# Kernel optimization log

Hardware: AMD Instinct MI355X
Metric: run time of the kernel (lower is better)

Reference implementation:

```python
import jax, jax.numpy as jnp
import numpy as np

B, L, HID = 1, 2048, 4096
H, KV, D = 32, 2, 128
ROT = int(D * 0.5)  # partial rotary dims per head
THETA = 10000.0
SCALE = D ** -0.5


def _rope_tables(L, rot, theta):
    inv_freq = 1.0 / (theta ** (np.arange(0, rot, 2, dtype=np.float32) / rot))  # [rot/2]
    t = np.arange(L, dtype=np.float32)
    freqs = np.outer(t, inv_freq)  # [L, rot/2]
    return jnp.asarray(np.cos(freqs)), jnp.asarray(np.sin(freqs))


def setup_inputs() -> dict:
    key = jax.random.key(0)
    ks = jax.random.split(key, 8)
    s = HID ** -0.5
    x = jax.random.normal(ks[0], (B, L, HID), dtype=jnp.float32)
    Wq = jax.random.normal(ks[1], (HID, H * D), dtype=jnp.float32) * s
    Wk = jax.random.normal(ks[2], (HID, KV * D), dtype=jnp.float32) * s
    Wv = jax.random.normal(ks[3], (HID, KV * D), dtype=jnp.float32) * s
    Wo = jax.random.normal(ks[4], (H * D, HID), dtype=jnp.float32) * s
    bq = jax.random.normal(ks[5], (H * D,), dtype=jnp.float32) * 0.01
    bk = jax.random.normal(ks[6], (KV * D,), dtype=jnp.float32) * 0.01
    bv = jax.random.normal(ks[7], (KV * D,), dtype=jnp.float32) * 0.01
    cos, sin = _rope_tables(L, ROT, THETA)
    # additive causal mask
    causal = jnp.tril(jnp.ones((L, L), dtype=bool))
    attention_mask = jnp.where(causal, 0.0, -1e9)[None, None].astype(jnp.float32)
    return {"x": x, "Wq": Wq, "bq": bq, "Wk": Wk, "bk": bk, "Wv": Wv, "bv": bv,
            "Wo": Wo, "cos": cos, "sin": sin, "attention_mask": attention_mask}


def _apply_rope(t, cos, sin):
    # t: [B, h, L, D]; rotary on first ROT dims, pass-through on the rest
    t_rot, t_pass = t[..., :ROT], t[..., ROT:]
    x1, x2 = t_rot[..., : ROT // 2], t_rot[..., ROT // 2:]
    c = cos[None, None]  # [1,1,L,ROT/2]
    s = sin[None, None]
    rot = jnp.concatenate([x1 * c - x2 * s, x2 * c + x1 * s], axis=-1)
    return jnp.concatenate([rot, t_pass], axis=-1)


def reference(x, Wq, bq, Wk, bk, Wv, bv, Wo, cos, sin, attention_mask):
    Bx, Lx, _ = x.shape
    q = (x @ Wq + bq).reshape(Bx, Lx, H, D).transpose(0, 2, 1, 3)   # [B,H,L,D]
    k = (x @ Wk + bk).reshape(Bx, Lx, KV, D).transpose(0, 2, 1, 3)  # [B,KV,L,D]
    v = (x @ Wv + bv).reshape(Bx, Lx, KV, D).transpose(0, 2, 1, 3)
    q = _apply_rope(q, cos, sin)
    k = _apply_rope(k, cos, sin)
    # GQA: repeat KV heads
    rep = H // KV
    k = jnp.repeat(k, rep, axis=1)  # [B,H,L,D]
    v = jnp.repeat(v, rep, axis=1)
    w = jnp.einsum('bhqd,bhkd->bhqk', q, k) * SCALE + attention_mask
    w = jax.nn.softmax(w, axis=-1)
    o = jnp.einsum('bhqk,bhkd->bhqd', w, v)
    o = o.transpose(0, 2, 1, 3).reshape(Bx, Lx, H * D)
    return o @ Wo
```

## Files before the change

kernel.cpp:

```cpp
#include <hip/hip_runtime.h>
#include <stdint.h>

#define L_SEQ 2048
#define HID   4096
#define NH    32
#define NKV   2
#define DH    128
#define NQKV  4608
#define QSCALE 0.088388347648318447f

typedef __bf16 bf16x8 __attribute__((ext_vector_type(8)));
typedef float  f32x4  __attribute__((ext_vector_type(4)));

__device__ __forceinline__ unsigned short f2bf(float f) {
  union { float f; unsigned u; } cv; cv.f = f;
  unsigned u = cv.u;
  return (unsigned short)((u + 0x7fffu + ((u >> 16) & 1u)) >> 16);
}
__device__ __forceinline__ float bf2f(unsigned short h) {
  union { unsigned u; float f; } cv; cv.u = (unsigned)h << 16; return cv.f;
}
__device__ __forceinline__ unsigned pk2(float a, float b) {
  return (unsigned)f2bf(a) | ((unsigned)f2bf(b) << 16);
}

#define GLL16(gsrc, ldst)                                                              \
  __builtin_amdgcn_global_load_lds(                                                    \
      (const __attribute__((address_space(1))) unsigned int*)(gsrc),                   \
      (__attribute__((address_space(3))) unsigned int*)(ldst), 16, 0, 0)

__device__ __forceinline__ void transpose_tile(const float* __restrict__ in,
                                               unsigned short* __restrict__ out,
                                               int R, int C, int bx, int by,
                                               float* tile , int tid) {
  const int c0 = bx * 64, r0 = by * 64;
  #pragma unroll
  for (int it = 0; it < 4; ++it) {
    int row = it * 16 + (tid >> 4);
    float4 v = *reinterpret_cast<const float4*>(&in[(size_t)(r0 + row) * C + c0 + (tid & 15) * 4]);
    tile[row * 65 + (tid & 15) * 4 + 0] = v.x;
    tile[row * 65 + (tid & 15) * 4 + 1] = v.y;
    tile[row * 65 + (tid & 15) * 4 + 2] = v.z;
    tile[row * 65 + (tid & 15) * 4 + 3] = v.w;
  }
  __syncthreads();
  #pragma unroll
  for (int it = 0; it < 8; ++it) {
    int c  = it * 8 + (tid >> 5);
    int rp = tid & 31;
    unsigned u = (unsigned)f2bf(tile[2 * rp * 65 + c]) |
                 ((unsigned)f2bf(tile[(2 * rp + 1) * 65 + c]) << 16);
    *reinterpret_cast<unsigned*>(&out[(size_t)(c0 + c) * R + r0 + 2 * rp]) = u;
  }
}

__global__ __launch_bounds__(256) void preproc_kernel(const float* __restrict__ x,
                                                      unsigned short* __restrict__ xb,
                                                      const float* __restrict__ Wq,
                                                      const float* __restrict__ Wk,
                                                      const float* __restrict__ Wv,
                                                      unsigned short* __restrict__ Wqkvt) {
  __shared__ __attribute__((aligned(16))) float tile[64 * 65];
  const int tid = threadIdx.x;
  int bid = blockIdx.x;
  if (bid < 8192) {
    int i = bid * 256 + tid;
    float4 v = reinterpret_cast<const float4*>(x)[i];
    ushort4 o;
    o.x = f2bf(v.x); o.y = f2bf(v.y); o.z = f2bf(v.z); o.w = f2bf(v.w);
    reinterpret_cast<ushort4*>(xb)[i] = o;
    return;
  }
  bid -= 8192;
  if (bid < 4096) {
    transpose_tile(Wq, Wqkvt, HID, HID, bid & 63, bid >> 6, tile, tid);
  } else if (bid < 4352) {
    bid -= 4096;
    transpose_tile(Wk, Wqkvt + (size_t)4096 * HID, HID, 256, bid & 3, bid >> 2, tile, tid);
  } else {
    bid -= 4352;
    transpose_tile(Wv, Wqkvt + (size_t)4352 * HID, HID, 256, bid & 3, bid >> 2, tile, tid);
  }
}

__global__ __launch_bounds__(256) void vtrans_kernel(const unsigned short* __restrict__ in,
                                                     unsigned short* __restrict__ out) {
  __shared__ unsigned short tile[64][72];
  const int l0 = blockIdx.x * 64, d0 = blockIdx.y * 64, g = blockIdx.z;
  const int tid = threadIdx.x;
  #pragma unroll
  for (int it = 0; it < 2; ++it) {
    int l = it * 32 + (tid >> 3);
    *reinterpret_cast<uint4*>(&tile[l][(tid & 7) * 8]) =
        *reinterpret_cast<const uint4*>(&in[((size_t)g * L_SEQ + l0 + l) * DH + d0 + (tid & 7) * 8]);
  }
  __syncthreads();
  #pragma unroll
  for (int it = 0; it < 2; ++it) {
    int d = it * 32 + (tid >> 3);
    unsigned short tmp[8];
    #pragma unroll
    for (int e = 0; e < 8; ++e) tmp[e] = tile[(tid & 7) * 8 + e][d];
    *reinterpret_cast<uint4*>(&out[((size_t)g * DH + d0 + d) * L_SEQ + l0 + (tid & 7) * 8]) =
        *reinterpret_cast<uint4*>(tmp);
  }
}

#define TBM 128
#define TBN 128
#define TBK 32

template <int MODE>
__global__ __launch_bounds__(256, 4) void gemm128_kernel(const unsigned short* __restrict__ A,
                                                         const unsigned short* __restrict__ Bt,
                                                         float* __restrict__ C,
                                                         const float* __restrict__ bq,
                                                         const float* __restrict__ bk,
                                                         const float* __restrict__ bv,
                                                         const float* __restrict__ cosT,
                                                         const float* __restrict__ sinT,
                                                         unsigned short* __restrict__ qb,
                                                         unsigned short* __restrict__ kb,
                                                         unsigned short* __restrict__ vlin,
                                                         const float* __restrict__ Wo,
                                                         unsigned short* __restrict__ Wot,
                                                         int M, int N, int K) {
  __shared__ __attribute__((aligned(16))) unsigned short smem[2 * TBM * TBK + 2 * TBN * TBK];
  const int tid = threadIdx.x;
  const int gx = N >> 7;
  const int nwgg = (M >> 7) * gx;
  const int flat = blockIdx.x;

  if (MODE == 1 && flat >= nwgg) {
    int tb = flat - nwgg;
    transpose_tile(Wo, Wot, HID, HID, tb & 63, tb >> 6,
                   reinterpret_cast<float*>(smem), tid);
    return;
  }

  unsigned short* Asb = smem;
  unsigned short* Bsb = smem + 2 * TBM * TBK;
  const int wave = tid >> 6, lane = tid & 63;
  const int lg = lane >> 4, ll = lane & 15;
  const int wm = wave >> 1, wn = wave & 1;

  int bx = flat % gx, by = flat / gx;
  if ((nwgg & 7) == 0) {
    int t = (flat & 7) * (nwgg >> 3) + (flat >> 3);
    bx = t % gx; by = t / gx;
  }
  const int m0 = by * TBM, n0 = bx * TBN;

  f32x4 acc[4][4] = {};
  const int NT = K >> 5;

  auto stage = [&](int t, int buf) {
    const int k0 = t * TBK;
    #pragma unroll
    for (int i = 0; i < 2; ++i) {
      int ci  = (i * 4 + wave) * 64 + lane;
      int row = ci >> 2;
      int cg  = (ci & 3) ^ ((row >> 1) & 3);
      GLL16(A + (size_t)(m0 + row) * K + k0 + cg * 8, &Asb[buf * TBM * TBK + (i * 4 + wave) * 512]);
    }
    #pragma unroll
    for (int i = 0; i < 2; ++i) {
      int ci  = (i * 4 + wave) * 64 + lane;
      int row = ci >> 2;
      int cg  = (ci & 3) ^ ((row >> 1) & 3);
      GLL16(Bt + (size_t)(n0 + row) * K + k0 + cg * 8, &Bsb[buf * TBN * TBK + (i * 4 + wave) * 512]);
    }
  };

  stage(0, 0);
  stage(1, 1);

  for (int t = 0; t < NT; ++t) {
    const int cur = t & 1;
    if (t + 1 < NT) asm volatile("s_waitcnt vmcnt(4)" ::: "memory");
    else            asm volatile("s_waitcnt vmcnt(0)" ::: "memory");
    __builtin_amdgcn_s_barrier();

    const unsigned short* Ac = &Asb[cur * TBM * TBK];
    const unsigned short* Bc = &Bsb[cur * TBN * TBK];
    bf16x8 afr[4], bfr[4];
    #pragma unroll
    for (int i = 0; i < 4; ++i) {
      int ra = wm * 64 + i * 16 + ll;
      afr[i] = *reinterpret_cast<const bf16x8*>(
          &Ac[ra * 32 + ((lg ^ ((ra >> 1) & 3)) * 8)]);
      int rb = wn * 64 + i * 16 + ll;
      bfr[i] = *reinterpret_cast<const bf16x8*>(
          &Bc[rb * 32 + ((lg ^ ((rb >> 1) & 3)) * 8)]);
    }
    asm volatile("s_waitcnt lgkmcnt(0)" ::: "memory");
    __builtin_amdgcn_s_barrier();
    if (t + 2 < NT) stage(t + 2, cur);

    __builtin_amdgcn_s_setprio(1);
    #pragma unroll
    for (int i = 0; i < 4; ++i)
      #pragma unroll
      for (int j = 0; j < 4; ++j)
        acc[i][j] = __builtin_amdgcn_mfma_f32_16x16x32_bf16(afr[i], bfr[j], acc[i][j], 0, 0, 0);
    __builtin_amdgcn_s_setprio(0);
  }

  if (MODE == 0) {
    #pragma unroll
    for (int i = 0; i < 4; ++i)
      #pragma unroll
      for (int j = 0; j < 4; ++j) {
        int col  = n0 + wn * 64 + j * 16 + ll;
        int rowb = m0 + wm * 64 + i * 16 + lg * 4;
        #pragma unroll
        for (int r = 0; r < 4; ++r)
          C[(size_t)(rowb + r) * N + col] = acc[i][j][r];
      }
  } else {
    const int region = (n0 < 4096) ? 0 : ((n0 < 4352) ? 1 : 2);
    const int hh = (region == 0) ? (n0 >> 7) : ((region == 1) ? ((n0 - 4096) >> 7) : ((n0 - 4352) >> 7));
    const float* bias = (region == 0) ? bq : ((region == 1) ? bk : bv);
    #pragma unroll
    for (int j = 0; j < 4; ++j) {
      float bj = bias[hh * DH + wn * 64 + j * 16 + ll];
      #pragma unroll
      for (int i = 0; i < 4; ++i)
        #pragma unroll
        for (int r = 0; r < 4; ++r) acc[i][j][r] += bj;
    }
    if (region < 2 && wn == 0) {
      #pragma unroll
      for (int i = 0; i < 4; ++i)
        #pragma unroll
        for (int r = 0; r < 4; ++r) {
          int l = m0 + wm * 64 + i * 16 + lg * 4 + r;
          float c0 = cosT[l * 32 + ll],      s0 = sinT[l * 32 + ll];
          float c1 = cosT[l * 32 + 16 + ll], s1 = sinT[l * 32 + 16 + ll];
          float x10 = acc[i][0][r], x20 = acc[i][2][r];
          float x11 = acc[i][1][r], x21 = acc[i][3][r];
          acc[i][0][r] = x10 * c0 - x20 * s0;
          acc[i][2][r] = x20 * c0 + x10 * s0;
          acc[i][1][r] = x11 * c1 - x21 * s1;
          acc[i][3][r] = x21 * c1 + x11 * s1;
        }
    }
    const float scale = (region == 0) ? QSCALE : 1.f;
    unsigned short* dst = (region == 0) ? qb : ((region == 1) ? kb : vlin);
    #pragma unroll
    for (int i = 0; i < 4; ++i)
      #pragma unroll
      for (int j = 0; j < 4; ++j) {
        int d = wn * 64 + j * 16 + ll;
        #pragma unroll
        for (int r = 0; r < 4; ++r) {
          int l = m0 + wm * 64 + i * 16 + lg * 4 + r;
          dst[((size_t)hh * L_SEQ + l) * DH + d] = f2bf(acc[i][j][r] * scale);
        }
      }
  }
}

__global__ __launch_bounds__(256, 2) void attn_kernel(const unsigned short* __restrict__ qg,
                                                      const unsigned short* __restrict__ kb,
                                                      const unsigned short* __restrict__ vt,
                                                      unsigned short* __restrict__ ob) {
  __shared__ __attribute__((aligned(16))) unsigned short Ks[2][64 * 128];
  __shared__ __attribute__((aligned(16))) unsigned short Vs[2][128 * 64];

  const int pair = blockIdx.x, h = blockIdx.y;
  const int g = h >> 4;
  const int tid = threadIdx.x, wave = tid >> 6, lane = tid & 63;
  const int lg = lane >> 4, ll = lane & 15;

  const int krow = (lane >> 4);
  const int kcg0 = (lane & 15);
  const int vrow = (lane >> 3);
  const int vcg0 = (lane & 7);

  #pragma unroll
  for (int seg = 0; seg < 2; ++seg) {
    const int qt = seg ? (31 - pair) : pair;
    const int q0 = qt * 64 + wave * 16;

    bf16x8 qf[4];
    #pragma unroll
    for (int f = 0; f < 4; ++f)
      qf[f] = *reinterpret_cast<const bf16x8*>(
          qg + ((size_t)h * L_SEQ + q0 + ll) * DH + f * 32 + lg * 8);

    f32x4 of[8] = {};
    float m = -1e30f, lsum = 0.f;

    const int kvN = qt + 1;
    int cur = 0;

    #pragma unroll
    for (int c = 0; c < 4; ++c) {
      int issue = wave * 4 + c;
      int rk = issue * 4 + krow;
      GLL16(kb + ((size_t)g * L_SEQ + rk) * DH + (kcg0 ^ (rk & 7)) * 8, &Ks[0][issue * 512]);
      int rv = issue * 8 + vrow;
      GLL16(vt + ((size_t)g * DH + rv) * L_SEQ + (vcg0 ^ (rv & 7)) * 8, &Vs[0][issue * 512]);
    }
    __syncthreads();

    for (int t = 0; t < kvN; ++t) {
      if (t + 1 < kvN) {
        int kv1 = (t + 1) * 64;
        #pragma unroll
        for (int c = 0; c < 4; ++c) {
          int issue = wave * 4 + c;
          int rk = issue * 4 + krow;
          GLL16(kb + ((size_t)g * L_SEQ + kv1 + rk) * DH + (kcg0 ^ (rk & 7)) * 8,
                &Ks[cur ^ 1][issue * 512]);
          int rv = issue * 8 + vrow;
          GLL16(vt + ((size_t)g * DH + rv) * L_SEQ + kv1 + (vcg0 ^ (rv & 7)) * 8,
                &Vs[cur ^ 1][issue * 512]);
        }
      }

      f32x4 s[4] = {};
      const unsigned short* Kc = &Ks[cur][0];
      #pragma unroll
      for (int cf = 0; cf < 4; ++cf) {
        bf16x8 kf[4];
        #pragma unroll
        for (int f = 0; f < 4; ++f) {
          int rk = cf * 16 + ll;
          int cc = (f * 4 + lg) ^ (rk & 7);
          kf[f] = *reinterpret_cast<const bf16x8*>(&Kc[rk * 128 + cc * 8]);
        }
        __builtin_amdgcn_s_setprio(1);
        #pragma unroll
        for (int f = 0; f < 4; ++f)
          s[cf] = __builtin_amdgcn_mfma_f32_16x16x32_bf16(kf[f], qf[f], s[cf], 0, 0, 0);
        __builtin_amdgcn_s_setprio(0);
      }

      if (t == qt) {
        #pragma unroll
        for (int cf = 0; cf < 4; ++cf)
          #pragma unroll
          for (int r = 0; r < 4; ++r)
            if (cf * 16 + lg * 4 + r > wave * 16 + ll) s[cf][r] = -1e30f;
      }

      float pmax = -1e30f;
      #pragma unroll
      for (int cf = 0; cf < 4; ++cf)
        #pragma unroll
        for (int r = 0; r < 4; ++r) pmax = fmaxf(pmax, s[cf][r]);
      if (!__all(pmax - m <= 8.f)) {
        float mx = fmaxf(pmax, __shfl_xor(pmax, 16));
        mx = fmaxf(mx, __shfl_xor(mx, 32));
        float mnew = fmaxf(m, mx);
        float alpha = __expf(m - mnew);
        m = mnew;
        lsum *= alpha;
        float af[4];
        #pragma unroll
        for (int r = 0; r < 4; ++r) af[r] = __shfl(alpha, lg * 4 + r);
        #pragma unroll
        for (int ds = 0; ds < 8; ++ds)
          #pragma unroll
          for (int r = 0; r < 4; ++r) of[ds][r] *= af[r];
      }

      unsigned wlo[4], whi[4];
      float psum = 0.f;
      #pragma unroll
      for (int cf = 0; cf < 4; ++cf) {
        float p0 = __expf(s[cf][0] - m), p1 = __expf(s[cf][1] - m);
        float p2 = __expf(s[cf][2] - m), p3 = __expf(s[cf][3] - m);
        psum += (p0 + p1) + (p2 + p3);
        wlo[cf] = pk2(p0, p1);
        whi[cf] = pk2(p2, p3);
      }
      lsum += psum;

      bf16x8 pa[2];
      {
        const int src0 = ((lg & 1) << 5) + ll;
        const int src1 = src0 + 16;
        const bool hi = (lg & 2) != 0;
        #pragma unroll
        for (int ks = 0; ks < 2; ++ks) {
          int e0a = __shfl((int)wlo[ks * 2], src0);
          int e1a = __shfl((int)whi[ks * 2], src0);
          int e2a = __shfl((int)wlo[ks * 2], src1);
          int e3a = __shfl((int)whi[ks * 2], src1);
          int e0b = __shfl((int)wlo[ks * 2 + 1], src0);
          int e1b = __shfl((int)whi[ks * 2 + 1], src0);
          int e2b = __shfl((int)wlo[ks * 2 + 1], src1);
          int e3b = __shfl((int)whi[ks * 2 + 1], src1);
          union { int i[4]; bf16x8 v; } u;
          u.i[0] = hi ? e0b : e0a;
          u.i[1] = hi ? e1b : e1a;
          u.i[2] = hi ? e2b : e2a;
          u.i[3] = hi ? e3b : e3a;
          pa[ks] = u.v;
        }
      }

      const unsigned short* Vc = &Vs[cur][0];
      #pragma unroll
      for (int ds = 0; ds < 8; ++ds) {
        bf16x8 vf[2];
        #pragma unroll
        for (int ks = 0; ks < 2; ++ks) {
          int dl = ds * 16 + ll;
          int cc = (ks * 4 + lg) ^ (dl & 7);
          vf[ks] = *reinterpret_cast<const bf16x8*>(&Vc[dl * 64 + cc * 8]);
        }
        __builtin_amdgcn_s_setprio(1);
        #pragma unroll
        for (int ks = 0; ks < 2; ++ks)
          of[ds] = __builtin_amdgcn_mfma_f32_16x16x32_bf16(pa[ks], vf[ks], of[ds], 0, 0, 0);
        __builtin_amdgcn_s_setprio(0);
      }

      __syncthreads();
      cur ^= 1;
    }

    float tot = lsum + __shfl_xor(lsum, 16);
    tot += __shfl_xor(tot, 32);
    float inv = 1.f / tot;
    float invr[4];
    #pragma unroll
    for (int r = 0; r < 4; ++r) invr[r] = __shfl(inv, lg * 4 + r);
    #pragma unroll
    for (int ds = 0; ds < 8; ++ds)
      #pragma unroll
      for (int r = 0; r < 4; ++r) {
        int row = q0 + lg * 4 + r;
        ob[(size_t)row * (NH * DH) + h * DH + ds * 16 + ll] = f2bf(of[ds][r] * invr[r]);
      }
    __syncthreads();
  }
}

extern "C" void kernel_launch(void* const* d_in, const int* in_sizes, int n_in,
                              void* d_out, int out_size, void* d_ws, size_t ws_size,
                              hipStream_t stream) {
  (void)in_sizes; (void)n_in; (void)out_size; (void)ws_size;
  const float* x    = (const float*)d_in[0];
  const float* Wq   = (const float*)d_in[1];
  const float* bq   = (const float*)d_in[2];
  const float* Wk   = (const float*)d_in[3];
  const float* bk   = (const float*)d_in[4];
  const float* Wv   = (const float*)d_in[5];
  const float* bv   = (const float*)d_in[6];
  const float* Wo   = (const float*)d_in[7];
  const float* cosT = (const float*)d_in[8];
  const float* sinT = (const float*)d_in[9];

  char* ws = (char*)d_ws;
  size_t off = 0;
  auto alloc = [&](size_t bytes) { void* p = ws + off; off += (bytes + 255) & ~(size_t)255; return p; };
  unsigned short* xb    = (unsigned short*)alloc((size_t)L_SEQ * HID * 2);
  unsigned short* Wqkvt = (unsigned short*)alloc((size_t)NQKV * HID * 2);
  unsigned short* Wot   = (unsigned short*)alloc((size_t)HID * HID * 2);
  unsigned short* qbuf  = (unsigned short*)alloc((size_t)NH * L_SEQ * DH * 2);
  unsigned short* kbuf  = (unsigned short*)alloc((size_t)NKV * L_SEQ * DH * 2);
  unsigned short* vlin  = (unsigned short*)alloc((size_t)NKV * L_SEQ * DH * 2);
  unsigned short* vtb   = (unsigned short*)alloc((size_t)NKV * DH * L_SEQ * 2);
  unsigned short* attno = (unsigned short*)alloc((size_t)L_SEQ * HID * 2);

  preproc_kernel<<<12800, 256, 0, stream>>>(x, xb, Wq, Wk, Wv, Wqkvt);

  gemm128_kernel<1><<<576 + 4096, 256, 0, stream>>>(
      xb, Wqkvt, nullptr, bq, bk, bv, cosT, sinT, qbuf, kbuf, vlin,
      Wo, Wot, L_SEQ, NQKV, HID);

  vtrans_kernel<<<dim3(L_SEQ / 64, DH / 64, NKV), 256, 0, stream>>>(vlin, vtb);

  attn_kernel<<<dim3(16, NH), 256, 0, stream>>>(qbuf, kbuf, vtb, attno);

  gemm128_kernel<0><<<512, 256, 0, stream>>>(
      attno, Wot, (float*)d_out, nullptr, nullptr, nullptr, nullptr, nullptr,
      nullptr, nullptr, nullptr, nullptr, nullptr, L_SEQ, HID, HID);
}
```

Before: 330.2 us.

## Split-K both GEMMs with bf16 partials and separate reduction epilogue kernels

Both projection GEMMs now run as split-K with two K halves, which doubles the number of workgroups. Each half writes its bf16 partials to a workspace, and new kernels sum the halves. One applies bias, RoPE and the Q scale for the QKV output; the other writes the final fp32 output. The Wo transpose moves from the first GEMM launch into the preprocessing kernel. This adds partial-buffer traffic and two extra launches. Rounding the partials to bf16 before the sum loses some precision.

```diff
diff --git a/kernel.cpp b/kernel.cpp
--- a/kernel.cpp
+++ b/kernel.cpp
@@ -59,7 +59,9 @@
                                                       const float* __restrict__ Wq,
                                                       const float* __restrict__ Wk,
                                                       const float* __restrict__ Wv,
-                                                      unsigned short* __restrict__ Wqkvt) {
+                                                      const float* __restrict__ Wo,
+                                                      unsigned short* __restrict__ Wqkvt,
+                                                      unsigned short* __restrict__ Wot) {
   __shared__ __attribute__((aligned(16))) float tile[64 * 65];
   const int tid = threadIdx.x;
   int bid = blockIdx.x;
@@ -77,9 +79,12 @@
   } else if (bid < 4352) {
     bid -= 4096;
     transpose_tile(Wk, Wqkvt + (size_t)4096 * HID, HID, 256, bid & 3, bid >> 2, tile, tid);
-  } else {
+  } else if (bid < 4608) {
     bid -= 4352;
     transpose_tile(Wv, Wqkvt + (size_t)4352 * HID, HID, 256, bid & 3, bid >> 2, tile, tid);
+  } else {
+    bid -= 4608;
+    transpose_tile(Wo, Wot, HID, HID, bid & 63, bid >> 6, tile, tid);
   }
 }
 
@@ -110,65 +115,46 @@
 #define TBN 128
 #define TBK 32
 
-template <int MODE>
-__global__ __launch_bounds__(256, 4) void gemm128_kernel(const unsigned short* __restrict__ A,
-                                                         const unsigned short* __restrict__ Bt,
-                                                         float* __restrict__ C,
-                                                         const float* __restrict__ bq,
-                                                         const float* __restrict__ bk,
-                                                         const float* __restrict__ bv,
-                                                         const float* __restrict__ cosT,
-                                                         const float* __restrict__ sinT,
-                                                         unsigned short* __restrict__ qb,
-                                                         unsigned short* __restrict__ kb,
-                                                         unsigned short* __restrict__ vlin,
-                                                         const float* __restrict__ Wo,
-                                                         unsigned short* __restrict__ Wot,
-                                                         int M, int N, int K) {
-  __shared__ __attribute__((aligned(16))) unsigned short smem[2 * TBM * TBK + 2 * TBN * TBK];
+__global__ __launch_bounds__(256, 4) void gemmsk_kernel(const unsigned short* __restrict__ A,
+                                                        const unsigned short* __restrict__ Bt,
+                                                        unsigned short* __restrict__ Cp,
+                                                        int M, int N, int K) {
+  __shared__ __attribute__((aligned(16))) unsigned short As[2][TBM * TBK];
+  __shared__ __attribute__((aligned(16))) unsigned short Bs[2][TBN * TBK];
   const int tid = threadIdx.x;
-  const int gx = N >> 7;
-  const int nwgg = (M >> 7) * gx;
-  const int flat = blockIdx.x;
-
-  if (MODE == 1 && flat >= nwgg) {
-    int tb = flat - nwgg;
-    transpose_tile(Wo, Wot, HID, HID, tb & 63, tb >> 6,
-                   reinterpret_cast<float*>(smem), tid);
-    return;
-  }
-
-  unsigned short* Asb = smem;
-  unsigned short* Bsb = smem + 2 * TBM * TBK;
   const int wave = tid >> 6, lane = tid & 63;
   const int lg = lane >> 4, ll = lane & 15;
   const int wm = wave >> 1, wn = wave & 1;
-
-  int bx = flat % gx, by = flat / gx;
-  if ((nwgg & 7) == 0) {
-    int t = (flat & 7) * (nwgg >> 3) + (flat >> 3);
+  const int kz = blockIdx.z;
+  const int kbase = kz * (K >> 1);
+  const int NT = K >> 6;
+
+  int gx = gridDim.x, nwg = gx * gridDim.y;
+  int flat = blockIdx.y * gx + blockIdx.x;
+  int bx = blockIdx.x, by = blockIdx.y;
+  if ((nwg & 7) == 0) {
+    int t = (flat & 7) * (nwg >> 3) + (flat >> 3);
     bx = t % gx; by = t / gx;
   }
   const int m0 = by * TBM, n0 = bx * TBN;
 
   f32x4 acc[4][4] = {};
-  const int NT = K >> 5;
 
   auto stage = [&](int t, int buf) {
-    const int k0 = t * TBK;
+    const int k0 = kbase + t * TBK;
     #pragma unroll
     for (int i = 0; i < 2; ++i) {
       int ci  = (i * 4 + wave) * 64 + lane;
       int row = ci >> 2;
       int cg  = (ci & 3) ^ ((row >> 1) & 3);
-      GLL16(A + (size_t)(m0 + row) * K + k0 + cg * 8, &Asb[buf * TBM * TBK + (i * 4 + wave) * 512]);
+      GLL16(A + (size_t)(m0 + row) * K + k0 + cg * 8, &As[buf][(i * 4 + wave) * 512]);
     }
     #pragma unroll
     for (int i = 0; i < 2; ++i) {
       int ci  = (i * 4 + wave) * 64 + lane;
       int row = ci >> 2;
       int cg  = (ci & 3) ^ ((row >> 1) & 3);
-      GLL16(Bt + (size_t)(n0 + row) * K + k0 + cg * 8, &Bsb[buf * TBN * TBK + (i * 4 + wave) * 512]);
+      GLL16(Bt + (size_t)(n0 + row) * K + k0 + cg * 8, &Bs[buf][(i * 4 + wave) * 512]);
     }
   };
 
@@ -181,8 +167,8 @@
     else            asm volatile("s_waitcnt vmcnt(0)" ::: "memory");
     __builtin_amdgcn_s_barrier();
 
-    const unsigned short* Ac = &Asb[cur * TBM * TBK];
-    const unsigned short* Bc = &Bsb[cur * TBN * TBK];
+    const unsigned short* Ac = &As[cur][0];
+    const unsigned short* Bc = &Bs[cur][0];
     bf16x8 afr[4], bfr[4];
     #pragma unroll
     for (int i = 0; i < 4; ++i) {
@@ -206,59 +192,76 @@
     __builtin_amdgcn_s_setprio(0);
   }
 
-  if (MODE == 0) {
-    #pragma unroll
-    for (int i = 0; i < 4; ++i)
-      #pragma unroll
-      for (int j = 0; j < 4; ++j) {
-        int col  = n0 + wn * 64 + j * 16 + ll;
-        int rowb = m0 + wm * 64 + i * 16 + lg * 4;
-        #pragma unroll
-        for (int r = 0; r < 4; ++r)
-          C[(size_t)(rowb + r) * N + col] = acc[i][j][r];
-      }
+  unsigned short* Cz = Cp + (size_t)kz * M * N;
+  #pragma unroll
+  for (int i = 0; i < 4; ++i)
+    #pragma unroll
+    for (int j = 0; j < 4; ++j) {
+      int col  = n0 + wn * 64 + j * 16 + ll;
+      int rowb = m0 + wm * 64 + i * 16 + lg * 4;
+      #pragma unroll
+      for (int r = 0; r < 4; ++r)
+        Cz[(size_t)(rowb + r) * N + col] = f2bf(acc[i][j][r]);
+    }
+}
+
+__global__ __launch_bounds__(128) void qkv_post_kernel(const unsigned short* __restrict__ qp,
+                                                       const float* __restrict__ bq,
+                                                       const float* __restrict__ bk,
+                                                       const float* __restrict__ bv,
+                                                       const float* __restrict__ cosT,
+                                                       const float* __restrict__ sinT,
+                                                       unsigned short* __restrict__ qb,
+                                                       unsigned short* __restrict__ kb,
+                                                       unsigned short* __restrict__ vlin) {
+  const unsigned short* p1 = qp + (size_t)L_SEQ * NQKV;
+  int l = blockIdx.x, y = blockIdx.y, d = threadIdx.x;
+  auto rd = [&](size_t idx) { return bf2f(qp[idx]) + bf2f(p1[idx]); };
+  if (y < 34) {
+    const bool isq = (y < 32);
+    const int hh = isq ? y : (y - 32);
+    const float* bias = isq ? bq : bk;
+    size_t base = (size_t)l * NQKV + (isq ? 0 : 4096) + hh * DH;
+    float v = rd(base + d) + bias[hh * DH + d];
+    float o;
+    if (d < 32) {
+      float x2 = rd(base + d + 32) + bias[hh * DH + d + 32];
+      o = v * cosT[l * 32 + d] - x2 * sinT[l * 32 + d];
+    } else if (d < 64) {
+      int i = d - 32;
+      float x1 = rd(base + i) + bias[hh * DH + i];
+      o = v * cosT[l * 32 + i] + x1 * sinT[l * 32 + i];
+    } else {
+      o = v;
+    }
+    if (isq) qb[((size_t)hh * L_SEQ + l) * DH + d] = f2bf(o * QSCALE);
+    else     kb[((size_t)hh * L_SEQ + l) * DH + d] = f2bf(o);
   } else {
-    const int region = (n0 < 4096) ? 0 : ((n0 < 4352) ? 1 : 2);
-    const int hh = (region == 0) ? (n0 >> 7) : ((region == 1) ? ((n0 - 4096) >> 7) : ((n0 - 4352) >> 7));
-    const float* bias = (region == 0) ? bq : ((region == 1) ? bk : bv);
-    #pragma unroll
-    for (int j = 0; j < 4; ++j) {
-      float bj = bias[hh * DH + wn * 64 + j * 16 + ll];
-      #pragma unroll
-      for (int i = 0; i < 4; ++i)
-        #pragma unroll
-        for (int r = 0; r < 4; ++r) acc[i][j][r] += bj;
-    }
-    if (region < 2 && wn == 0) {
-      #pragma unroll
-      for (int i = 0; i < 4; ++i)
-        #pragma unroll
-        for (int r = 0; r < 4; ++r) {
-          int l = m0 + wm * 64 + i * 16 + lg * 4 + r;
-          float c0 = cosT[l * 32 + ll],      s0 = sinT[l * 32 + ll];
-          float c1 = cosT[l * 32 + 16 + ll], s1 = sinT[l * 32 + 16 + ll];
-          float x10 = acc[i][0][r], x20 = acc[i][2][r];
-          float x11 = acc[i][1][r], x21 = acc[i][3][r];
-          acc[i][0][r] = x10 * c0 - x20 * s0;
-          acc[i][2][r] = x20 * c0 + x10 * s0;
-          acc[i][1][r] = x11 * c1 - x21 * s1;
-          acc[i][3][r] = x21 * c1 + x11 * s1;
-        }
-    }
-    const float scale = (region == 0) ? QSCALE : 1.f;
-    unsigned short* dst = (region == 0) ? qb : ((region == 1) ? kb : vlin);
-    #pragma unroll
-    for (int i = 0; i < 4; ++i)
-      #pragma unroll
-      for (int j = 0; j < 4; ++j) {
-        int d = wn * 64 + j * 16 + ll;
-        #pragma unroll
-        for (int r = 0; r < 4; ++r) {
-          int l = m0 + wm * 64 + i * 16 + lg * 4 + r;
-          dst[((size_t)hh * L_SEQ + l) * DH + d] = f2bf(acc[i][j][r] * scale);
-        }
-      }
-  }
+    int g = y - 34;
+    float o = rd((size_t)l * NQKV + 4352 + g * DH + d) + bv[g * DH + d];
+    vlin[((size_t)g * L_SEQ + l) * DH + d] = f2bf(o);
+  }
+}
+
+__global__ __launch_bounds__(256) void oreduce_kernel(const unsigned short* __restrict__ op,
+                                                      float* __restrict__ out) {
+  const size_t n = (size_t)L_SEQ * HID;
+  size_t i = (size_t)blockIdx.x * 256 + threadIdx.x;
+  uint4 u0 = reinterpret_cast<const uint4*>(op)[i];
+  uint4 u1 = reinterpret_cast<const uint4*>(op + n)[i];
+  float o[8];
+  unsigned a[4] = {u0.x, u0.y, u0.z, u0.w}, b[4] = {u1.x, u1.y, u1.z, u1.w};
+  #pragma unroll
+  for (int k = 0; k < 4; ++k) {
+    union { unsigned u; float f; } lo0, hi0, lo1, hi1;
+    lo0.u = a[k] << 16;         lo1.u = b[k] << 16;
+    hi0.u = a[k] & 0xffff0000u; hi1.u = b[k] & 0xffff0000u;
+    o[k * 2]     = lo0.f + lo1.f;
+    o[k * 2 + 1] = hi0.f + hi1.f;
+  }
+  float4* dst = reinterpret_cast<float4*>(out + i * 8);
+  dst[0] = make_float4(o[0], o[1], o[2], o[3]);
+  dst[1] = make_float4(o[4], o[5], o[6], o[7]);
 }
 
 __global__ __launch_bounds__(256, 2) void attn_kernel(const unsigned short* __restrict__ qg,
@@ -459,26 +462,31 @@
   char* ws = (char*)d_ws;
   size_t off = 0;
   auto alloc = [&](size_t bytes) { void* p = ws + off; off += (bytes + 255) & ~(size_t)255; return p; };
-  unsigned short* xb    = (unsigned short*)alloc((size_t)L_SEQ * HID * 2);
-  unsigned short* Wqkvt = (unsigned short*)alloc((size_t)NQKV * HID * 2);
-  unsigned short* Wot   = (unsigned short*)alloc((size_t)HID * HID * 2);
-  unsigned short* qbuf  = (unsigned short*)alloc((size_t)NH * L_SEQ * DH * 2);
-  unsigned short* kbuf  = (unsigned short*)alloc((size_t)NKV * L_SEQ * DH * 2);
-  unsigned short* vlin  = (unsigned short*)alloc((size_t)NKV * L_SEQ * DH * 2);
-  unsigned short* vtb   = (unsigned short*)alloc((size_t)NKV * DH * L_SEQ * 2);
-  unsigned short* attno = (unsigned short*)alloc((size_t)L_SEQ * HID * 2);
-
-  preproc_kernel<<<12800, 256, 0, stream>>>(x, xb, Wq, Wk, Wv, Wqkvt);
-
-  gemm128_kernel<1><<<576 + 4096, 256, 0, stream>>>(
-      xb, Wqkvt, nullptr, bq, bk, bv, cosT, sinT, qbuf, kbuf, vlin,
-      Wo, Wot, L_SEQ, NQKV, HID);
+  unsigned short* xb      = (unsigned short*)alloc((size_t)L_SEQ * HID * 2);
+  unsigned short* Wqkvt   = (unsigned short*)alloc((size_t)NQKV * HID * 2);
+  unsigned short* Wot     = (unsigned short*)alloc((size_t)HID * HID * 2);
+  unsigned short* qkvpart = (unsigned short*)alloc((size_t)2 * L_SEQ * NQKV * 2);
+  unsigned short* qbuf    = (unsigned short*)alloc((size_t)NH * L_SEQ * DH * 2);
+  unsigned short* kbuf    = (unsigned short*)alloc((size_t)NKV * L_SEQ * DH * 2);
+  unsigned short* vlin    = (unsigned short*)alloc((size_t)NKV * L_SEQ * DH * 2);
+  unsigned short* vtb     = (unsigned short*)alloc((size_t)NKV * DH * L_SEQ * 2);
+  unsigned short* attno   = (unsigned short*)alloc((size_t)L_SEQ * HID * 2);
+  unsigned short* opart   = qkvpart;
+
+  preproc_kernel<<<16896, 256, 0, stream>>>(x, xb, Wq, Wk, Wv, Wo, Wqkvt, Wot);
+
+  gemmsk_kernel<<<dim3(NQKV / TBN, L_SEQ / TBM, 2), 256, 0, stream>>>(
+      xb, Wqkvt, qkvpart, L_SEQ, NQKV, HID);
+
+  qkv_post_kernel<<<dim3(L_SEQ, 36), 128, 0, stream>>>(qkvpart, bq, bk, bv, cosT, sinT,
+                                                       qbuf, kbuf, vlin);
 
   vtrans_kernel<<<dim3(L_SEQ / 64, DH / 64, NKV), 256, 0, stream>>>(vlin, vtb);
 
   attn_kernel<<<dim3(16, NH), 256, 0, stream>>>(qbuf, kbuf, vtb, attno);
 
-  gemm128_kernel<0><<<512, 256, 0, stream>>>(
-      attno, Wot, (float*)d_out, nullptr, nullptr, nullptr, nullptr, nullptr,
-      nullptr, nullptr, nullptr, nullptr, nullptr, L_SEQ, HID, HID);
-}
+  gemmsk_kernel<<<dim3(HID / TBN, L_SEQ / TBM, 2), 256, 0, stream>>>(
+      attno, Wot, opart, L_SEQ, HID, HID);
+
+  oreduce_kernel<<<(L_SEQ * HID / 8) / 256, 256, 0, stream>>>(opart, (float*)d_out);
+}
```

Result: slower. 370.4 us (+12.2%).

## Enlarge GEMM tile to 256x128 with 8 waves and move Wo transpose to preproc

Applied to the files above, without the earlier changes.

The GEMM kernel now uses 256x128 output tiles with 512 threads (8 waves) instead of 128x128 with 256 threads, so more reuse of each B tile per load and fewer workgroups. The Wo transpose moves out of the QKV GEMM launch into the preprocessing kernel, which simplifies the GEMM's block mapping to a 2D grid. Risks: the larger tile gives fewer workgroups (288 and 256), which may underfill the 256 CUs and unbalance waves, and higher LDS use per block lowers occupancy.

```diff
diff --git a/kernel.cpp b/kernel.cpp
--- a/kernel.cpp
+++ b/kernel.cpp
@@ -59,7 +59,9 @@
                                                       const float* __restrict__ Wq,
                                                       const float* __restrict__ Wk,
                                                       const float* __restrict__ Wv,
-                                                      unsigned short* __restrict__ Wqkvt) {
+                                                      const float* __restrict__ Wo,
+                                                      unsigned short* __restrict__ Wqkvt,
+                                                      unsigned short* __restrict__ Wot) {
   __shared__ __attribute__((aligned(16))) float tile[64 * 65];
   const int tid = threadIdx.x;
   int bid = blockIdx.x;
@@ -77,9 +79,12 @@
   } else if (bid < 4352) {
     bid -= 4096;
     transpose_tile(Wk, Wqkvt + (size_t)4096 * HID, HID, 256, bid & 3, bid >> 2, tile, tid);
-  } else {
+  } else if (bid < 4608) {
     bid -= 4352;
     transpose_tile(Wv, Wqkvt + (size_t)4352 * HID, HID, 256, bid & 3, bid >> 2, tile, tid);
+  } else {
+    bid -= 4608;
+    transpose_tile(Wo, Wot, HID, HID, bid & 63, bid >> 6, tile, tid);
   }
 }
 
@@ -106,12 +111,12 @@
   }
 }
 
-#define TBM 128
+#define TBM 256
 #define TBN 128
 #define TBK 32
 
 template <int MODE>
-__global__ __launch_bounds__(256, 4) void gemm128_kernel(const unsigned short* __restrict__ A,
+__global__ __launch_bounds__(512, 4) void gemm256_kernel(const unsigned short* __restrict__ A,
                                                          const unsigned short* __restrict__ Bt,
                                                          float* __restrict__ C,
                                                          const float* __restrict__ bq,
@@ -122,31 +127,19 @@
                                                          unsigned short* __restrict__ qb,
                                                          unsigned short* __restrict__ kb,
                                                          unsigned short* __restrict__ vlin,
-                                                         const float* __restrict__ Wo,
-                                                         unsigned short* __restrict__ Wot,
                                                          int M, int N, int K) {
-  __shared__ __attribute__((aligned(16))) unsigned short smem[2 * TBM * TBK + 2 * TBN * TBK];
+  __shared__ __attribute__((aligned(16))) unsigned short As[2][TBM * TBK];
+  __shared__ __attribute__((aligned(16))) unsigned short Bs[2][TBN * TBK];
   const int tid = threadIdx.x;
-  const int gx = N >> 7;
-  const int nwgg = (M >> 7) * gx;
-  const int flat = blockIdx.x;
-
-  if (MODE == 1 && flat >= nwgg) {
-    int tb = flat - nwgg;
-    transpose_tile(Wo, Wot, HID, HID, tb & 63, tb >> 6,
-                   reinterpret_cast<float*>(smem), tid);
-    return;
-  }
-
-  unsigned short* Asb = smem;
-  unsigned short* Bsb = smem + 2 * TBM * TBK;
   const int wave = tid >> 6, lane = tid & 63;
   const int lg = lane >> 4, ll = lane & 15;
   const int wm = wave >> 1, wn = wave & 1;
 
-  int bx = flat % gx, by = flat / gx;
-  if ((nwgg & 7) == 0) {
-    int t = (flat & 7) * (nwgg >> 3) + (flat >> 3);
+  int gx = gridDim.x, nwg = gx * gridDim.y;
+  int flat = blockIdx.y * gx + blockIdx.x;
+  int bx = blockIdx.x, by = blockIdx.y;
+  if ((nwg & 7) == 0) {
+    int t = (flat & 7) * (nwg >> 3) + (flat >> 3);
     bx = t % gx; by = t / gx;
   }
   const int m0 = by * TBM, n0 = bx * TBN;
@@ -158,17 +151,16 @@
     const int k0 = t * TBK;
     #pragma unroll
     for (int i = 0; i < 2; ++i) {
-      int ci  = (i * 4 + wave) * 64 + lane;
+      int ci  = (wave * 2 + i) * 64 + lane;
       int row = ci >> 2;
       int cg  = (ci & 3) ^ ((row >> 1) & 3);
-      GLL16(A + (size_t)(m0 + row) * K + k0 + cg * 8, &Asb[buf * TBM * TBK + (i * 4 + wave) * 512]);
-    }
-    #pragma unroll
-    for (int i = 0; i < 2; ++i) {
-      int ci  = (i * 4 + wave) * 64 + lane;
+      GLL16(A + (size_t)(m0 + row) * K + k0 + cg * 8, &As[buf][(wave * 2 + i) * 512]);
+    }
+    {
+      int ci  = wave * 64 + lane;
       int row = ci >> 2;
       int cg  = (ci & 3) ^ ((row >> 1) & 3);
-      GLL16(Bt + (size_t)(n0 + row) * K + k0 + cg * 8, &Bsb[buf * TBN * TBK + (i * 4 + wave) * 512]);
+      GLL16(Bt + (size_t)(n0 + row) * K + k0 + cg * 8, &Bs[buf][wave * 512]);
     }
   };
 
@@ -177,12 +169,12 @@
 
   for (int t = 0; t < NT; ++t) {
     const int cur = t & 1;
-    if (t + 1 < NT) asm volatile("s_waitcnt vmcnt(4)" ::: "memory");
+    if (t + 1 < NT) asm volatile("s_waitcnt vmcnt(3)" ::: "memory");
     else            asm volatile("s_waitcnt vmcnt(0)" ::: "memory");
     __builtin_amdgcn_s_barrier();
 
-    const unsigned short* Ac = &Asb[cur * TBM * TBK];
-    const unsigned short* Bc = &Bsb[cur * TBN * TBK];
+    const unsigned short* Ac = &As[cur][0];
+    const unsigned short* Bc = &Bs[cur][0];
     bf16x8 afr[4], bfr[4];
     #pragma unroll
     for (int i = 0; i < 4; ++i) {
@@ -468,17 +460,16 @@
   unsigned short* vtb   = (unsigned short*)alloc((size_t)NKV * DH * L_SEQ * 2);
   unsigned short* attno = (unsigned short*)alloc((size_t)L_SEQ * HID * 2);
 
-  preproc_kernel<<<12800, 256, 0, stream>>>(x, xb, Wq, Wk, Wv, Wqkvt);
-
-  gemm128_kernel<1><<<576 + 4096, 256, 0, stream>>>(
-      xb, Wqkvt, nullptr, bq, bk, bv, cosT, sinT, qbuf, kbuf, vlin,
-      Wo, Wot, L_SEQ, NQKV, HID);
+  preproc_kernel<<<16896, 256, 0, stream>>>(x, xb, Wq, Wk, Wv, Wo, Wqkvt, Wot);
+
+  gemm256_kernel<1><<<dim3(NQKV / TBN, L_SEQ / TBM), 512, 0, stream>>>(
+      xb, Wqkvt, nullptr, bq, bk, bv, cosT, sinT, qbuf, kbuf, vlin, L_SEQ, NQKV, HID);
 
   vtrans_kernel<<<dim3(L_SEQ / 64, DH / 64, NKV), 256, 0, stream>>>(vlin, vtb);
 
   attn_kernel<<<dim3(16, NH), 256, 0, stream>>>(qbuf, kbuf, vtb, attno);
 
-  gemm128_kernel<0><<<512, 256, 0, stream>>>(
+  gemm256_kernel<0><<<dim3(HID / TBN, L_SEQ / TBM), 512, 0, stream>>>(
       attno, Wot, (float*)d_out, nullptr, nullptr, nullptr, nullptr, nullptr,
-      nullptr, nullptr, nullptr, nullptr, nullptr, L_SEQ, HID, HID);
-}
+      nullptr, nullptr, nullptr, L_SEQ, HID, HID);
+}
```

Measured after the change: 312.0 us. 1.06x faster.
